# Optimization experiments

Hardware: AMD Instinct MI355X
Metric: run time of the kernel (lower is better)

## Reference

```python
import jax, jax.numpy as jnp
import numpy as np

N = 100000   # nodes
E = 1600000  # edges
D_IN = 128
H = 64
L = 3        # num SAGE layers
G = 512      # graphs in batch


def setup_inputs() -> dict:
    key = jax.random.key(0)
    ks = jax.random.split(key, 12)
    s = 0.05
    return {
        "x": jax.random.normal(ks[0], (N, D_IN), dtype=jnp.float32),
        "edge_index": jax.random.randint(ks[1], (2, E), 0, N, dtype=jnp.int64),
        "edge_attr": jax.random.normal(ks[2], (E, 1), dtype=jnp.float32),
        "batch": jnp.sort(jax.random.randint(ks[3], (N,), 0, G, dtype=jnp.int64)),
        "W0": jax.random.normal(ks[4], (D_IN, H), dtype=jnp.float32) * s,
        "b0": jnp.zeros((H,), dtype=jnp.float32),
        "Wl": jax.random.normal(ks[5], (L, H, H), dtype=jnp.float32) * s,  # lin_l (aggregated neighbors), has bias
        "bl": jnp.zeros((L, H), dtype=jnp.float32),
        "Wr": jax.random.normal(ks[6], (L, H, H), dtype=jnp.float32) * s,  # lin_r (root), no bias
        "W1": jax.random.normal(ks[7], (H, H), dtype=jnp.float32) * s,
        "b1": jnp.zeros((H,), dtype=jnp.float32),
    }


def reference(x, edge_index, edge_attr, batch, W0, b0, Wl, bl, Wr, W1, b1):
    # edge_attr is accepted but unused, matching the torch module.
    h = jax.nn.relu(x @ W0 + b0)                    # [N, H]
    src, dst = edge_index[0], edge_index[1]
    ones_e = jnp.ones((E,), dtype=h.dtype)
    deg = jax.ops.segment_sum(ones_e, dst, num_segments=N)
    deg = jnp.clip(deg, 1.0)[:, None]               # avoid div by zero (PyG mean -> 0 for isolated)
    for i in range(L):
        # SAGEConv: mean-aggregate source features onto targets, then lin_l(agg)+lin_r(h)
        agg = jax.ops.segment_sum(h[src], dst, num_segments=N) / deg  # [N, H]
        h = jax.nn.relu(agg @ Wl[i] + bl[i] + h @ Wr[i])
    # global_mean_pool over batch ids
    cnt = jax.ops.segment_sum(jnp.ones((N,), dtype=h.dtype), batch, num_segments=G)
    pooled = jax.ops.segment_sum(h, batch, num_segments=G) / jnp.clip(cnt, 1.0)[:, None]  # [G, H]
    return pooled @ W1 + b1                          # [G, H]
```

## Files before the change

### kernel.cpp

```cpp
#include <hip/hip_runtime.h>
#include <hip/hip_bf16.h>

#define NN 100000
#define NE 1600000
#define DIN 128
#define NG 512
#define MAXD 64
#define NBUK 391
#define BCAP 5120
#define CHUNK ((NE + NBUK - 1) / NBUK)
#define NTILE ((NN + 63) >> 6)

typedef __attribute__((ext_vector_type(8))) __bf16 bf16x8;
typedef __attribute__((ext_vector_type(4))) float f32x4;

static __device__ __forceinline__ unsigned short bfhi(float f) {
    __hip_bfloat16 h = __float2bfloat16(f);
    return *reinterpret_cast<unsigned short*>(&h);
}
static __device__ __forceinline__ float bf2f(unsigned short u) {
    unsigned v = (unsigned)u << 16;
    return __uint_as_float(v);
}
static __device__ __forceinline__ bf16x8 ldfrag(const unsigned short* p) {
    bf16x8 r;
    __builtin_memcpy(&r, p, 16);
    return r;
}


#define GB 256
__global__ void __launch_bounds__(512) k_front(const int* __restrict__ src,
                                               const int* __restrict__ dst,
                                               int* __restrict__ cursor,
                                               unsigned int* __restrict__ bucket,
                                               const float* __restrict__ x,
                                               const float* __restrict__ W0,
                                               const float* __restrict__ b0,
                                               float* __restrict__ h) {
    __shared__ unsigned short sA0[16 * 64 * 8];
    __shared__ unsigned short sA1[16 * 64 * 8];
    __shared__ unsigned short sB0[16 * 64 * 8];
    __shared__ unsigned short sB1[16 * 64 * 8];
    __shared__ int lcnt[NBUK];
    __shared__ int lbase[NBUK];
    if (blockIdx.x < NBUK) {
        for (int i = threadIdx.x; i < NBUK; i += 512) lcnt[i] = 0;
        __syncthreads();
        int e0 = blockIdx.x * CHUNK;
        int e1 = min(e0 + CHUNK, NE);
        for (int e = e0 + (int)threadIdx.x; e < e1; e += 512)
            atomicAdd(&lcnt[dst[e] >> 8], 1);
        __syncthreads();
        for (int i = threadIdx.x; i < NBUK; i += 512) {
            int c = lcnt[i];
            lbase[i] = c ? atomicAdd(&cursor[i], c) : 0;
            lcnt[i] = 0;
        }
        __syncthreads();
        for (int e = e0 + (int)threadIdx.x; e < e1; e += 512) {
            int d = dst[e];
            int s = src[e];
            int bk = d >> 8;
            int pos = lbase[bk] + atomicAdd(&lcnt[bk], 1);
            if (pos < BCAP)
                bucket[(size_t)bk * BCAP + pos] = ((unsigned)s << 8) | (unsigned)(d & 255);
        }
    } else {
        for (int i = threadIdx.x; i < 8192; i += 512) {
            int k = i >> 6, c = i & 63;
            int slot = ((k >> 5) << 2) | (c >> 4);
            int ln   = (((k >> 3) & 3) << 4) | (c & 15);
            int addr = (((slot << 6) | ln) << 3) | (k & 7);
            float w0 = W0[i];
            unsigned short hh = bfhi(w0);
            sB0[addr] = hh;
            sB1[addr] = bfhi(w0 - bf2f(hh));
        }
        int lane = threadIdx.x & 63;
        int wv   = threadIdx.x >> 6;
        int cb   = wv & 3;
        int rbh  = wv >> 2;
        int col  = (cb << 4) | (lane & 15);
        float bj = b0[col];
        int r0   = (lane >> 4) << 2;
        for (int t = blockIdx.x - NBUK; t < NTILE; t += GB) {
            int n0 = t << 6;
            __syncthreads();
#pragma unroll
            for (int i = 0; i < 4; ++i) {
                int tau = (int)threadIdx.x + (i << 9);
                int r = tau >> 5, kq = tau & 31;
                int n = n0 + r;
                float4 v = make_float4(0.f, 0.f, 0.f, 0.f);
                if (n < NN) v = *(const float4*)(x + ((size_t)n << 7) + (kq << 2));
                int k0   = kq << 2;
                int slot = ((k0 >> 5) << 2) | (r >> 4);
                int ln   = (((k0 >> 3) & 3) << 4) | (r & 15);
                int base = (((slot << 6) | ln) << 3) | (k0 & 7);
                unsigned short h0 = bfhi(v.x), h1 = bfhi(v.y),
                               h2 = bfhi(v.z), h3 = bfhi(v.w);
                *(ushort4*)(&sA0[base]) = make_ushort4(h0, h1, h2, h3);
                *(ushort4*)(&sA1[base]) = make_ushort4(
                    bfhi(v.x - bf2f(h0)), bfhi(v.y - bf2f(h1)),
                    bfhi(v.z - bf2f(h2)), bfhi(v.w - bf2f(h3)));
            }
            __syncthreads();
            f32x4 acc[2] = {{0.f,0.f,0.f,0.f},{0.f,0.f,0.f,0.f}};
#pragma unroll
            for (int ks = 0; ks < 4; ++ks) {
                int bbase = ((((ks << 2) | cb) << 6) | lane) << 3;
                bf16x8 bh = ldfrag(&sB0[bbase]);
                bf16x8 bl_ = ldfrag(&sB1[bbase]);
#pragma unroll
                for (int rl = 0; rl < 2; ++rl) {
                    int rb = (rbh << 1) | rl;
                    int abase = ((((ks << 2) | rb) << 6) | lane) << 3;
                    bf16x8 ah = ldfrag(&sA0[abase]);
                    bf16x8 al = ldfrag(&sA1[abase]);
                    acc[rl] = __builtin_amdgcn_mfma_f32_16x16x32_bf16(ah, bh,  acc[rl], 0, 0, 0);
                    acc[rl] = __builtin_amdgcn_mfma_f32_16x16x32_bf16(ah, bl_, acc[rl], 0, 0, 0);
                    acc[rl] = __builtin_amdgcn_mfma_f32_16x16x32_bf16(al, bh,  acc[rl], 0, 0, 0);
                }
            }
#pragma unroll
            for (int rl = 0; rl < 2; ++rl) {
                int rb = (rbh << 1) | rl;
#pragma unroll
                for (int reg = 0; reg < 4; ++reg) {
                    int row = (rb << 4) + r0 + reg;
                    int n = n0 + row;
                    if (n < NN)
                        h[((size_t)n << 6) + col] = fmaxf(acc[rl][reg] + bj, 0.f);
                }
            }
        }
    }
}

__device__ __forceinline__ void gemmLR_mfma(unsigned short* sA0, unsigned short* sA1,
                                            unsigned short* sBL0, unsigned short* sBL1,
                                            unsigned short* sBR0, unsigned short* sBR1,
                                            int tid, int nblk, int bidx,
                                            float* __restrict__ h_r,
                                            __hip_bfloat16* __restrict__ g,
                                            const float* __restrict__ Wl,
                                            const float* __restrict__ bl,
                                            const float* __restrict__ Wr) {
    for (int i = tid; i < 4096; i += 256) {
        int k = i >> 6, c = i & 63;
        int slot = ((k >> 5) << 2) | (c >> 4);
        int ln   = (((k >> 3) & 3) << 4) | (c & 15);
        int addr = (((slot << 6) | ln) << 3) | (k & 7);
        float wl = Wl[i];
        unsigned short hl = bfhi(wl);
        sBL0[addr] = hl;
        sBL1[addr] = bfhi(wl - bf2f(hl));
        float wr = Wr[i];
        unsigned short hr = bfhi(wr);
        sBR0[addr] = hr;
        sBR1[addr] = bfhi(wr - bf2f(hr));
    }
    int lane = tid & 63;
    int cb   = tid >> 6;
    int col  = (cb << 4) | (lane & 15);
    float bj = bl[col];
    int r0   = (lane >> 4) << 2;
    unsigned short* gp = (unsigned short*)g;
    for (int t = bidx; t < NTILE; t += nblk) {
        int n0 = t << 6;
        __syncthreads();
#pragma unroll
        for (int i = 0; i < 4; ++i) {
            int tau = tid + (i << 8);
            int r = tau >> 4, kq = tau & 15;
            int n = n0 + r;
            float4 v = make_float4(0.f, 0.f, 0.f, 0.f);
            if (n < NN) v = *(const float4*)(h_r + ((size_t)n << 6) + (kq << 2));
            int k0   = kq << 2;
            int slot = ((k0 >> 5) << 2) | (r >> 4);
            int ln   = (((k0 >> 3) & 3) << 4) | (r & 15);
            int base = (((slot << 6) | ln) << 3) | (k0 & 7);
            unsigned short h0 = bfhi(v.x), h1 = bfhi(v.y),
                           h2 = bfhi(v.z), h3 = bfhi(v.w);
            *(ushort4*)(&sA0[base]) = make_ushort4(h0, h1, h2, h3);
            *(ushort4*)(&sA1[base]) = make_ushort4(
                bfhi(v.x - bf2f(h0)), bfhi(v.y - bf2f(h1)),
                bfhi(v.z - bf2f(h2)), bfhi(v.w - bf2f(h3)));
        }
        __syncthreads();
        f32x4 accl[4] = {{0.f,0.f,0.f,0.f},{0.f,0.f,0.f,0.f},
                         {0.f,0.f,0.f,0.f},{0.f,0.f,0.f,0.f}};
        f32x4 accr[4] = {{0.f,0.f,0.f,0.f},{0.f,0.f,0.f,0.f},
                         {0.f,0.f,0.f,0.f},{0.f,0.f,0.f,0.f}};
#pragma unroll
        for (int ks = 0; ks < 2; ++ks) {
            int bbase = ((((ks << 2) | cb) << 6) | lane) << 3;
            bf16x8 bLh = ldfrag(&sBL0[bbase]);
            bf16x8 bLl = ldfrag(&sBL1[bbase]);
            bf16x8 bRh = ldfrag(&sBR0[bbase]);
            bf16x8 bRl = ldfrag(&sBR1[bbase]);
#pragma unroll
            for (int rb = 0; rb < 4; ++rb) {
                int abase = ((((ks << 2) | rb) << 6) | lane) << 3;
                bf16x8 ah = ldfrag(&sA0[abase]);
                bf16x8 al = ldfrag(&sA1[abase]);
                accl[rb] = __builtin_amdgcn_mfma_f32_16x16x32_bf16(ah, bLh, accl[rb], 0, 0, 0);
                accl[rb] = __builtin_amdgcn_mfma_f32_16x16x32_bf16(ah, bLl, accl[rb], 0, 0, 0);
                accl[rb] = __builtin_amdgcn_mfma_f32_16x16x32_bf16(al, bLh, accl[rb], 0, 0, 0);
                accr[rb] = __builtin_amdgcn_mfma_f32_16x16x32_bf16(ah, bRh, accr[rb], 0, 0, 0);
                accr[rb] = __builtin_amdgcn_mfma_f32_16x16x32_bf16(ah, bRl, accr[rb], 0, 0, 0);
                accr[rb] = __builtin_amdgcn_mfma_f32_16x16x32_bf16(al, bRh, accr[rb], 0, 0, 0);
            }
        }
#pragma unroll
        for (int rb = 0; rb < 4; ++rb) {
#pragma unroll
            for (int reg = 0; reg < 4; ++reg) {
                int row = (rb << 4) + r0 + reg;
                int n = n0 + row;
                if (n < NN) {
                    size_t o = ((size_t)n << 6) + col;
                    gp[o]  = bfhi(accl[rb][reg]);
                    h_r[o] = accr[rb][reg] + bj;
                }
            }
        }
    }
}

#define MGB 512
__global__ void __launch_bounds__(256) k_mid(const unsigned int* __restrict__ bucket,
                                             const int* __restrict__ cursor,
                                             int* __restrict__ cnt,
                                             int* __restrict__ ell,
                                             float* __restrict__ h_r,
                                             __hip_bfloat16* __restrict__ g,
                                             const float* __restrict__ Wl,
                                             const float* __restrict__ bl,
                                             const float* __restrict__ Wr) {
    __shared__ unsigned short sA0[8 * 64 * 8];
    __shared__ unsigned short sA1[8 * 64 * 8];
    __shared__ unsigned short sBL0[8 * 64 * 8];
    __shared__ unsigned short sBL1[8 * 64 * 8];
    __shared__ unsigned short sBR0[8 * 64 * 8];
    __shared__ unsigned short sBR1[8 * 64 * 8];
    __shared__ int lc[256];
    if (blockIdx.x < NBUK) {
        lc[threadIdx.x] = 0;
        int b = blockIdx.x;
        int4* ep = (int4*)(ell + (((size_t)b << 8) * MAXD));
        for (int i = threadIdx.x; i < (256 * MAXD) / 4; i += 256)
            ep[i] = make_int4(NN, NN, NN, NN);
        __syncthreads();
        int m = min(cursor[b], BCAP);
        const unsigned int* bp = bucket + (size_t)b * BCAP;
        for (int i = threadIdx.x; i < m; i += 256) {
            unsigned v = bp[i];
            int dlo = (int)(v & 255u);
            int s   = (int)(v >> 8);
            int p   = atomicAdd(&lc[dlo], 1);
            if (p < MAXD)
                ell[(((size_t)b << 8) + dlo) * MAXD + p] = s;
        }
        __syncthreads();
        int n = (b << 8) + (int)threadIdx.x;
        if (n < NN) cnt[n] = lc[threadIdx.x];
    } else {
        gemmLR_mfma(sA0, sA1, sBL0, sBL1, sBR0, sBR1,
                    threadIdx.x, MGB, blockIdx.x - NBUK, h_r, g, Wl, bl, Wr);
    }
}

__global__ void __launch_bounds__(256) k_gemmLR(float* __restrict__ h_r,
                                                __hip_bfloat16* __restrict__ g,
                                                const float* __restrict__ Wl,
                                                const float* __restrict__ bl,
                                                const float* __restrict__ Wr) {
    __shared__ unsigned short sA0[8 * 64 * 8];
    __shared__ unsigned short sA1[8 * 64 * 8];
    __shared__ unsigned short sBL0[8 * 64 * 8];
    __shared__ unsigned short sBL1[8 * 64 * 8];
    __shared__ unsigned short sBR0[8 * 64 * 8];
    __shared__ unsigned short sBR1[8 * 64 * 8];
    gemmLR_mfma(sA0, sA1, sBL0, sBL1, sBR0, sBR1,
                threadIdx.x, gridDim.x, blockIdx.x, h_r, g, Wl, bl, Wr);
}

__global__ void __launch_bounds__(256) k_gather(const unsigned int* __restrict__ g2,
                                                float* __restrict__ r_h,
                                                const int* __restrict__ cnt,
                                                const int* __restrict__ ell) {
    int lane = threadIdx.x & 63;
    int half = lane >> 5;
    int col  = lane & 31;
    int wv = __builtin_amdgcn_readfirstlane((int)((blockIdx.x * 256 + threadIdx.x) >> 6));
    int nw = (gridDim.x * 256) >> 6;
    for (int p = wv; p < NN / 2; p += nw) {
        int nA = 2 * p, nB = nA + 1;
        int dgA = cnt[nA], dgB = cnt[nB];
        int myn  = half ? nB : nA;
        int mydg = half ? dgB : dgA;
        int maxd = min(max(dgA, dgB), MAXD);
        int iters = (maxd + 7) & ~7;
        int idx0 = ell[(size_t)myn * MAXD + col];
        int idx1 = NN;
        if (iters > 32) idx1 = ell[(size_t)myn * MAXD + 32 + col];
        float L0=0.f,L1=0.f,L2=0.f,L3=0.f,L4=0.f,L5=0.f,L6=0.f,L7=0.f;
        float H0=0.f,H1=0.f,H2=0.f,H3=0.f,H4=0.f,H5=0.f,H6=0.f,H7=0.f;
        int it0 = min(iters, 32);
        for (int j = 0; j < it0; j += 8) {
            int i0 = __shfl(idx0, half * 32 + j);
            int i1 = __shfl(idx0, half * 32 + j + 1);
            int i2 = __shfl(idx0, half * 32 + j + 2);
            int i3 = __shfl(idx0, half * 32 + j + 3);
            int i4 = __shfl(idx0, half * 32 + j + 4);
            int i5 = __shfl(idx0, half * 32 + j + 5);
            int i6 = __shfl(idx0, half * 32 + j + 6);
            int i7 = __shfl(idx0, half * 32 + j + 7);
            unsigned u0 = g2[(size_t)i0 * 32 + col];
            unsigned u1 = g2[(size_t)i1 * 32 + col];
            unsigned u2 = g2[(size_t)i2 * 32 + col];
            unsigned u3 = g2[(size_t)i3 * 32 + col];
            unsigned u4 = g2[(size_t)i4 * 32 + col];
            unsigned u5 = g2[(size_t)i5 * 32 + col];
            unsigned u6 = g2[(size_t)i6 * 32 + col];
            unsigned u7 = g2[(size_t)i7 * 32 + col];
            L0 += __uint_as_float(u0 << 16); H0 += __uint_as_float(u0 & 0xffff0000u);
            L1 += __uint_as_float(u1 << 16); H1 += __uint_as_float(u1 & 0xffff0000u);
            L2 += __uint_as_float(u2 << 16); H2 += __uint_as_float(u2 & 0xffff0000u);
            L3 += __uint_as_float(u3 << 16); H3 += __uint_as_float(u3 & 0xffff0000u);
            L4 += __uint_as_float(u4 << 16); H4 += __uint_as_float(u4 & 0xffff0000u);
            L5 += __uint_as_float(u5 << 16); H5 += __uint_as_float(u5 & 0xffff0000u);
            L6 += __uint_as_float(u6 << 16); H6 += __uint_as_float(u6 & 0xffff0000u);
            L7 += __uint_as_float(u7 << 16); H7 += __uint_as_float(u7 & 0xffff0000u);
        }
        for (int j = 0; j < iters - 32; j += 8) {
            int i0 = __shfl(idx1, half * 32 + j);
            int i1 = __shfl(idx1, half * 32 + j + 1);
            int i2 = __shfl(idx1, half * 32 + j + 2);
            int i3 = __shfl(idx1, half * 32 + j + 3);
            int i4 = __shfl(idx1, half * 32 + j + 4);
            int i5 = __shfl(idx1, half * 32 + j + 5);
            int i6 = __shfl(idx1, half * 32 + j + 6);
            int i7 = __shfl(idx1, half * 32 + j + 7);
            unsigned u0 = g2[(size_t)i0 * 32 + col];
            unsigned u1 = g2[(size_t)i1 * 32 + col];
            unsigned u2 = g2[(size_t)i2 * 32 + col];
            unsigned u3 = g2[(size_t)i3 * 32 + col];
            unsigned u4 = g2[(size_t)i4 * 32 + col];
            unsigned u5 = g2[(size_t)i5 * 32 + col];
            unsigned u6 = g2[(size_t)i6 * 32 + col];
            unsigned u7 = g2[(size_t)i7 * 32 + col];
            L0 += __uint_as_float(u0 << 16); H0 += __uint_as_float(u0 & 0xffff0000u);
            L1 += __uint_as_float(u1 << 16); H1 += __uint_as_float(u1 & 0xffff0000u);
            L2 += __uint_as_float(u2 << 16); H2 += __uint_as_float(u2 & 0xffff0000u);
            L3 += __uint_as_float(u3 << 16); H3 += __uint_as_float(u3 & 0xffff0000u);
            L4 += __uint_as_float(u4 << 16); H4 += __uint_as_float(u4 & 0xffff0000u);
            L5 += __uint_as_float(u5 << 16); H5 += __uint_as_float(u5 & 0xffff0000u);
            L6 += __uint_as_float(u6 << 16); H6 += __uint_as_float(u6 & 0xffff0000u);
            L7 += __uint_as_float(u7 << 16); H7 += __uint_as_float(u7 & 0xffff0000u);
        }
        float inv  = 1.0f / fmaxf((float)mydg, 1.0f);
        float sumL = ((L0 + L1) + (L2 + L3)) + ((L4 + L5) + (L6 + L7));
        float sumH = ((H0 + H1) + (H2 + H3)) + ((H4 + H5) + (H6 + H7));
        float2* rp = (float2*)r_h + (size_t)myn * 32 + col;
        float2 rv = *rp;
        rv.x = fmaxf(fmaf(sumL, inv, rv.x), 0.0f);
        rv.y = fmaxf(fmaf(sumH, inv, rv.y), 0.0f);
        *rp = rv;
    }
}

__global__ void __launch_bounds__(256) k_pool(const int* __restrict__ batch,
                                              const float* __restrict__ h,
                                              float* __restrict__ pool,
                                              float* __restrict__ cntg) {
    int lane = threadIdx.x & 63;
    int wid  = (blockIdx.x * 256 + threadIdx.x) >> 6;
    int nw   = (gridDim.x * 256) >> 6;
    int chunk = (NN + nw - 1) / nw;
    int n0 = wid * chunk;
    if (n0 >= NN) return;
    int n1 = min(n0 + chunk, NN);
    int cur = batch[n0];
    float acc = 0.0f, acc_c = 0.0f;
    for (int n = n0; n < n1; ++n) {
        int b = batch[n];
        if (b != cur) {
            atomicAdd(&pool[(size_t)cur * 64 + lane], acc);
            if (lane == 0) atomicAdd(&cntg[cur], acc_c);
            acc = 0.0f; acc_c = 0.0f; cur = b;
        }
        acc   += h[(size_t)n * 64 + lane];
        acc_c += 1.0f;
    }
    atomicAdd(&pool[(size_t)cur * 64 + lane], acc);
    if (lane == 0) atomicAdd(&cntg[cur], acc_c);
}

__global__ void __launch_bounds__(256) k_out(const float* __restrict__ pool,
                                             const float* __restrict__ cntg,
                                             const float* __restrict__ W1,
                                             const float* __restrict__ b1,
                                             float* __restrict__ out) {
    __shared__ float sW[64 * 64];
    for (int i = threadIdx.x; i < 64 * 64; i += 256) sW[i] = W1[i];
    __syncthreads();
    int lane = threadIdx.x & 63;
    int wid  = (blockIdx.x * 256 + threadIdx.x) >> 6;
    int nw   = (gridDim.x * 256) >> 6;
    for (int gidx = wid; gidx < NG; gidx += nw) {
        float ic = 1.0f / fmaxf(cntg[gidx], 1.0f);
        float acc = 0.0f;
#pragma unroll
        for (int k = 0; k < 64; ++k)
            acc = fmaf(pool[(size_t)gidx * 64 + k], sW[k * 64 + lane], acc);
        out[(size_t)gidx * 64 + lane] = fmaf(acc, ic, b1[lane]);
    }
}

extern "C" void kernel_launch(void* const* d_in, const int* in_sizes, int n_in,
                              void* d_out, int out_size, void* d_ws, size_t ws_size,
                              hipStream_t stream) {
    const float* x     = (const float*)d_in[0];
    const int*   ei    = (const int*)d_in[1];
    const int*   batch = (const int*)d_in[3];
    const float* W0    = (const float*)d_in[4];
    const float* b0    = (const float*)d_in[5];
    const float* Wl    = (const float*)d_in[6];
    const float* bl    = (const float*)d_in[7];
    const float* Wr    = (const float*)d_in[8];
    const float* W1    = (const float*)d_in[9];
    const float* b1    = (const float*)d_in[10];
    float* out = (float*)d_out;

    char* ws = (char*)d_ws;
    size_t off = 0;
    auto alloc = [&](size_t bytes) -> void* {
        void* p = ws + off;
        off += (bytes + 255) & ~(size_t)255;
        return p;
    };
    float*          A      = (float*)alloc((size_t)NN * 64 * 4);
    __hip_bfloat16* G      = (__hip_bfloat16*)alloc((size_t)NN * 64 * 2);
    size_t zstart = off;
    (void)alloc((size_t)MAXD * 2);
    int*   cursor = (int*)alloc((size_t)NBUK * 4);
    float* pool   = (float*)alloc((size_t)NG * 64 * 4);
    float* cntg   = (float*)alloc((size_t)NG * 4);
    size_t zlen = off - zstart;
    int*          ell    = (int*)alloc((size_t)NBUK * 256 * MAXD * 4);
    unsigned int* bucket = (unsigned int*)alloc((size_t)NBUK * BCAP * 4);
    int*          cnt    = (int*)alloc((size_t)NN * 4);

    const int* src = ei;
    const int* dst = ei + NE;

    hipMemsetAsync(ws + zstart, 0, zlen, stream);

    k_front<<<NBUK + GB, 512, 0, stream>>>(src, dst, cursor, bucket, x, W0, b0, A);
    k_mid<<<NBUK + MGB, 256, 0, stream>>>(bucket, cursor, cnt, ell, A, G,
                                          Wl, bl, Wr);
    k_gather<<<4096, 256, 0, stream>>>((const unsigned int*)G, A, cnt, ell);

    for (int l = 1; l < 3; ++l) {
        k_gemmLR<<<512, 256, 0, stream>>>(A, G,
                                          Wl + (size_t)l * 64 * 64,
                                          bl + (size_t)l * 64,
                                          Wr + (size_t)l * 64 * 64);
        k_gather<<<4096, 256, 0, stream>>>((const unsigned int*)G, A, cnt, ell);
    }

    k_pool<<<256, 256, 0, stream>>>(batch, A, pool, cntg);
    k_out<<<128, 256, 0, stream>>>(pool, cntg, W1, b1, out);
}
```

Measured before the change: 388.3 us.

## Swizzle LDS MFMA fragments and gather four nodes per wave with 8-byte loads

```diff
diff --git a/kernel.cpp b/kernel.cpp
--- a/kernel.cpp
+++ b/kernel.cpp
@@ -22,10 +22,13 @@
     unsigned v = (unsigned)u << 16;
     return __uint_as_float(v);
 }
-static __device__ __forceinline__ bf16x8 ldfrag(const unsigned short* p) {
+static __device__ __forceinline__ bf16x8 ldfrag(const void* p) {
     bf16x8 r;
     __builtin_memcpy(&r, p, 16);
     return r;
+}
+static __device__ __forceinline__ int swz(int a) {
+    return a ^ (((a >> 8) & 3) << 5) ^ (((a >> 12) & 3) << 4);
 }
 
 
@@ -71,11 +74,11 @@
             int k = i >> 6, c = i & 63;
             int slot = ((k >> 5) << 2) | (c >> 4);
             int ln   = (((k >> 3) & 3) << 4) | (c & 15);
-            int addr = (((slot << 6) | ln) << 3) | (k & 7);
+            int ba   = swz((((((slot << 6) | ln) << 3) | (k & 7)) << 1));
             float w0 = W0[i];
             unsigned short hh = bfhi(w0);
-            sB0[addr] = hh;
-            sB1[addr] = bfhi(w0 - bf2f(hh));
+            *(unsigned short*)((char*)sB0 + ba) = hh;
+            *(unsigned short*)((char*)sB1 + ba) = bfhi(w0 - bf2f(hh));
         }
         int lane = threadIdx.x & 63;
         int wv   = threadIdx.x >> 6;
@@ -97,11 +100,11 @@
                 int k0   = kq << 2;
                 int slot = ((k0 >> 5) << 2) | (r >> 4);
                 int ln   = (((k0 >> 3) & 3) << 4) | (r & 15);
-                int base = (((slot << 6) | ln) << 3) | (k0 & 7);
+                int ba   = swz((((((slot << 6) | ln) << 3) | (k0 & 7)) << 1));
                 unsigned short h0 = bfhi(v.x), h1 = bfhi(v.y),
                                h2 = bfhi(v.z), h3 = bfhi(v.w);
-                *(ushort4*)(&sA0[base]) = make_ushort4(h0, h1, h2, h3);
-                *(ushort4*)(&sA1[base]) = make_ushort4(
+                *(ushort4*)((char*)sA0 + ba) = make_ushort4(h0, h1, h2, h3);
+                *(ushort4*)((char*)sA1 + ba) = make_ushort4(
                     bfhi(v.x - bf2f(h0)), bfhi(v.y - bf2f(h1)),
                     bfhi(v.z - bf2f(h2)), bfhi(v.w - bf2f(h3)));
             }
@@ -109,15 +112,15 @@
             f32x4 acc[2] = {{0.f,0.f,0.f,0.f},{0.f,0.f,0.f,0.f}};
 #pragma unroll
             for (int ks = 0; ks < 4; ++ks) {
-                int bbase = ((((ks << 2) | cb) << 6) | lane) << 3;
-                bf16x8 bh = ldfrag(&sB0[bbase]);
-                bf16x8 bl_ = ldfrag(&sB1[bbase]);
+                int bb = swz(((((ks << 2) | cb) << 6) | lane) << 4);
+                bf16x8 bh  = ldfrag((const char*)sB0 + bb);
+                bf16x8 bl_ = ldfrag((const char*)sB1 + bb);
 #pragma unroll
                 for (int rl = 0; rl < 2; ++rl) {
                     int rb = (rbh << 1) | rl;
-                    int abase = ((((ks << 2) | rb) << 6) | lane) << 3;
-                    bf16x8 ah = ldfrag(&sA0[abase]);
-                    bf16x8 al = ldfrag(&sA1[abase]);
+                    int ab = swz(((((ks << 2) | rb) << 6) | lane) << 4);
+                    bf16x8 ah = ldfrag((const char*)sA0 + ab);
+                    bf16x8 al = ldfrag((const char*)sA1 + ab);
                     acc[rl] = __builtin_amdgcn_mfma_f32_16x16x32_bf16(ah, bh,  acc[rl], 0, 0, 0);
                     acc[rl] = __builtin_amdgcn_mfma_f32_16x16x32_bf16(ah, bl_, acc[rl], 0, 0, 0);
                     acc[rl] = __builtin_amdgcn_mfma_f32_16x16x32_bf16(al, bh,  acc[rl], 0, 0, 0);
@@ -151,15 +154,15 @@
         int k = i >> 6, c = i & 63;
         int slot = ((k >> 5) << 2) | (c >> 4);
         int ln   = (((k >> 3) & 3) << 4) | (c & 15);
-        int addr = (((slot << 6) | ln) << 3) | (k & 7);
+        int ba   = swz((((((slot << 6) | ln) << 3) | (k & 7)) << 1));
         float wl = Wl[i];
         unsigned short hl = bfhi(wl);
-        sBL0[addr] = hl;
-        sBL1[addr] = bfhi(wl - bf2f(hl));
+        *(unsigned short*)((char*)sBL0 + ba) = hl;
+        *(unsigned short*)((char*)sBL1 + ba) = bfhi(wl - bf2f(hl));
         float wr = Wr[i];
         unsigned short hr = bfhi(wr);
-        sBR0[addr] = hr;
-        sBR1[addr] = bfhi(wr - bf2f(hr));
+        *(unsigned short*)((char*)sBR0 + ba) = hr;
+        *(unsigned short*)((char*)sBR1 + ba) = bfhi(wr - bf2f(hr));
     }
     int lane = tid & 63;
     int cb   = tid >> 6;
@@ -180,11 +183,11 @@
             int k0   = kq << 2;
             int slot = ((k0 >> 5) << 2) | (r >> 4);
             int ln   = (((k0 >> 3) & 3) << 4) | (r & 15);
-            int base = (((slot << 6) | ln) << 3) | (k0 & 7);
+            int ba   = swz((((((slot << 6) | ln) << 3) | (k0 & 7)) << 1));
             unsigned short h0 = bfhi(v.x), h1 = bfhi(v.y),
                            h2 = bfhi(v.z), h3 = bfhi(v.w);
-            *(ushort4*)(&sA0[base]) = make_ushort4(h0, h1, h2, h3);
-            *(ushort4*)(&sA1[base]) = make_ushort4(
+            *(ushort4*)((char*)sA0 + ba) = make_ushort4(h0, h1, h2, h3);
+            *(ushort4*)((char*)sA1 + ba) = make_ushort4(
                 bfhi(v.x - bf2f(h0)), bfhi(v.y - bf2f(h1)),
                 bfhi(v.z - bf2f(h2)), bfhi(v.w - bf2f(h3)));
         }
@@ -195,16 +198,16 @@
                          {0.f,0.f,0.f,0.f},{0.f,0.f,0.f,0.f}};
 #pragma unroll
         for (int ks = 0; ks < 2; ++ks) {
-            int bbase = ((((ks << 2) | cb) << 6) | lane) << 3;
-            bf16x8 bLh = ldfrag(&sBL0[bbase]);
-            bf16x8 bLl = ldfrag(&sBL1[bbase]);
-            bf16x8 bRh = ldfrag(&sBR0[bbase]);
-            bf16x8 bRl = ldfrag(&sBR1[bbase]);
+            int bb = swz(((((ks << 2) | cb) << 6) | lane) << 4);
+            bf16x8 bLh = ldfrag((const char*)sBL0 + bb);
+            bf16x8 bLl = ldfrag((const char*)sBL1 + bb);
+            bf16x8 bRh = ldfrag((const char*)sBR0 + bb);
+            bf16x8 bRl = ldfrag((const char*)sBR1 + bb);
 #pragma unroll
             for (int rb = 0; rb < 4; ++rb) {
-                int abase = ((((ks << 2) | rb) << 6) | lane) << 3;
-                bf16x8 ah = ldfrag(&sA0[abase]);
-                bf16x8 al = ldfrag(&sA1[abase]);
+                int ab = swz(((((ks << 2) | rb) << 6) | lane) << 4);
+                bf16x8 ah = ldfrag((const char*)sA0 + ab);
+                bf16x8 al = ldfrag((const char*)sA1 + ab);
                 accl[rb] = __builtin_amdgcn_mfma_f32_16x16x32_bf16(ah, bLh, accl[rb], 0, 0, 0);
                 accl[rb] = __builtin_amdgcn_mfma_f32_16x16x32_bf16(ah, bLl, accl[rb], 0, 0, 0);
                 accl[rb] = __builtin_amdgcn_mfma_f32_16x16x32_bf16(al, bLh, accl[rb], 0, 0, 0);
@@ -287,87 +290,68 @@
                 threadIdx.x, gridDim.x, blockIdx.x, h_r, g, Wl, bl, Wr);
 }
 
-__global__ void __launch_bounds__(256) k_gather(const unsigned int* __restrict__ g2,
+__global__ void __launch_bounds__(256) k_gather(const uint2* __restrict__ g2,
                                                 float* __restrict__ r_h,
                                                 const int* __restrict__ cnt,
                                                 const int* __restrict__ ell) {
     int lane = threadIdx.x & 63;
-    int half = lane >> 5;
-    int col  = lane & 31;
+    int q    = lane >> 4;
+    int c16  = lane & 15;
     int wv = __builtin_amdgcn_readfirstlane((int)((blockIdx.x * 256 + threadIdx.x) >> 6));
     int nw = (gridDim.x * 256) >> 6;
-    for (int p = wv; p < NN / 2; p += nw) {
-        int nA = 2 * p, nB = nA + 1;
-        int dgA = cnt[nA], dgB = cnt[nB];
-        int myn  = half ? nB : nA;
-        int mydg = half ? dgB : dgA;
-        int maxd = min(max(dgA, dgB), MAXD);
+    for (int p = wv; p < NN / 4; p += nw) {
+        int n0  = 4 * p;
+        int myn = n0 + q;
+        int d   = cnt[myn];
+        int dm  = max(d, __shfl_xor(d, 16));
+        dm      = max(dm, __shfl_xor(dm, 32));
+        int maxd  = min(dm, MAXD);
         int iters = (maxd + 7) & ~7;
-        int idx0 = ell[(size_t)myn * MAXD + col];
-        int idx1 = NN;
-        if (iters > 32) idx1 = ell[(size_t)myn * MAXD + 32 + col];
-        float L0=0.f,L1=0.f,L2=0.f,L3=0.f,L4=0.f,L5=0.f,L6=0.f,L7=0.f;
-        float H0=0.f,H1=0.f,H2=0.f,H3=0.f,H4=0.f,H5=0.f,H6=0.f,H7=0.f;
-        int it0 = min(iters, 32);
-        for (int j = 0; j < it0; j += 8) {
-            int i0 = __shfl(idx0, half * 32 + j);
-            int i1 = __shfl(idx0, half * 32 + j + 1);
-            int i2 = __shfl(idx0, half * 32 + j + 2);
-            int i3 = __shfl(idx0, half * 32 + j + 3);
-            int i4 = __shfl(idx0, half * 32 + j + 4);
-            int i5 = __shfl(idx0, half * 32 + j + 5);
-            int i6 = __shfl(idx0, half * 32 + j + 6);
-            int i7 = __shfl(idx0, half * 32 + j + 7);
-            unsigned u0 = g2[(size_t)i0 * 32 + col];
-            unsigned u1 = g2[(size_t)i1 * 32 + col];
-            unsigned u2 = g2[(size_t)i2 * 32 + col];
-            unsigned u3 = g2[(size_t)i3 * 32 + col];
-            unsigned u4 = g2[(size_t)i4 * 32 + col];
-            unsigned u5 = g2[(size_t)i5 * 32 + col];
-            unsigned u6 = g2[(size_t)i6 * 32 + col];
-            unsigned u7 = g2[(size_t)i7 * 32 + col];
-            L0 += __uint_as_float(u0 << 16); H0 += __uint_as_float(u0 & 0xffff0000u);
-            L1 += __uint_as_float(u1 << 16); H1 += __uint_as_float(u1 & 0xffff0000u);
-            L2 += __uint_as_float(u2 << 16); H2 += __uint_as_float(u2 & 0xffff0000u);
-            L3 += __uint_as_float(u3 << 16); H3 += __uint_as_float(u3 & 0xffff0000u);
-            L4 += __uint_as_float(u4 << 16); H4 += __uint_as_float(u4 & 0xffff0000u);
-            L5 += __uint_as_float(u5 << 16); H5 += __uint_as_float(u5 & 0xffff0000u);
-            L6 += __uint_as_float(u6 << 16); H6 += __uint_as_float(u6 & 0xffff0000u);
-            L7 += __uint_as_float(u7 << 16); H7 += __uint_as_float(u7 & 0xffff0000u);
-        }
-        for (int j = 0; j < iters - 32; j += 8) {
-            int i0 = __shfl(idx1, half * 32 + j);
-            int i1 = __shfl(idx1, half * 32 + j + 1);
-            int i2 = __shfl(idx1, half * 32 + j + 2);
-            int i3 = __shfl(idx1, half * 32 + j + 3);
-            int i4 = __shfl(idx1, half * 32 + j + 4);
-            int i5 = __shfl(idx1, half * 32 + j + 5);
-            int i6 = __shfl(idx1, half * 32 + j + 6);
-            int i7 = __shfl(idx1, half * 32 + j + 7);
-            unsigned u0 = g2[(size_t)i0 * 32 + col];
-            unsigned u1 = g2[(size_t)i1 * 32 + col];
-            unsigned u2 = g2[(size_t)i2 * 32 + col];
-            unsigned u3 = g2[(size_t)i3 * 32 + col];
-            unsigned u4 = g2[(size_t)i4 * 32 + col];
-            unsigned u5 = g2[(size_t)i5 * 32 + col];
-            unsigned u6 = g2[(size_t)i6 * 32 + col];
-            unsigned u7 = g2[(size_t)i7 * 32 + col];
-            L0 += __uint_as_float(u0 << 16); H0 += __uint_as_float(u0 & 0xffff0000u);
-            L1 += __uint_as_float(u1 << 16); H1 += __uint_as_float(u1 & 0xffff0000u);
-            L2 += __uint_as_float(u2 << 16); H2 += __uint_as_float(u2 & 0xffff0000u);
-            L3 += __uint_as_float(u3 << 16); H3 += __uint_as_float(u3 & 0xffff0000u);
-            L4 += __uint_as_float(u4 << 16); H4 += __uint_as_float(u4 & 0xffff0000u);
-            L5 += __uint_as_float(u5 << 16); H5 += __uint_as_float(u5 & 0xffff0000u);
-            L6 += __uint_as_float(u6 << 16); H6 += __uint_as_float(u6 & 0xffff0000u);
-            L7 += __uint_as_float(u7 << 16); H7 += __uint_as_float(u7 & 0xffff0000u);
-        }
-        float inv  = 1.0f / fmaxf((float)mydg, 1.0f);
-        float sumL = ((L0 + L1) + (L2 + L3)) + ((L4 + L5) + (L6 + L7));
-        float sumH = ((H0 + H1) + (H2 + H3)) + ((H4 + H5) + (H6 + H7));
-        float2* rp = (float2*)r_h + (size_t)myn * 32 + col;
-        float2 rv = *rp;
-        rv.x = fmaxf(fmaf(sumL, inv, rv.x), 0.0f);
-        rv.y = fmaxf(fmaf(sumH, inv, rv.y), 0.0f);
+        int4 ld = *(const int4*)(ell + ((size_t)myn << 6) + (c16 << 2));
+        float a0=0.f, a1=0.f, a2=0.f, a3=0.f;
+        float e0=0.f, e1=0.f, e2=0.f, e3=0.f;
+        for (int j0 = 0; j0 < iters; j0 += 8) {
+            int s0 = (q << 4) | (j0 >> 2);
+            int i0 = __shfl(ld.x, s0);
+            int i1 = __shfl(ld.y, s0);
+            int i2 = __shfl(ld.z, s0);
+            int i3 = __shfl(ld.w, s0);
+            int i4 = __shfl(ld.x, s0 + 1);
+            int i5 = __shfl(ld.y, s0 + 1);
+            int i6 = __shfl(ld.z, s0 + 1);
+            int i7 = __shfl(ld.w, s0 + 1);
+            uint2 u0 = g2[(size_t)i0 * 16 + c16];
+            uint2 u1 = g2[(size_t)i1 * 16 + c16];
+            uint2 u2 = g2[(size_t)i2 * 16 + c16];
+            uint2 u3 = g2[(size_t)i3 * 16 + c16];
+            uint2 u4 = g2[(size_t)i4 * 16 + c16];
+            uint2 u5 = g2[(size_t)i5 * 16 + c16];
+            uint2 u6 = g2[(size_t)i6 * 16 + c16];
+            uint2 u7 = g2[(size_t)i7 * 16 + c16];
+            a0 += __uint_as_float(u0.x << 16); a1 += __uint_as_float(u0.x & 0xffff0000u);
+            a2 += __uint_as_float(u0.y << 16); a3 += __uint_as_float(u0.y & 0xffff0000u);
+            e0 += __uint_as_float(u1.x << 16); e1 += __uint_as_float(u1.x & 0xffff0000u);
+            e2 += __uint_as_float(u1.y << 16); e3 += __uint_as_float(u1.y & 0xffff0000u);
+            a0 += __uint_as_float(u2.x << 16); a1 += __uint_as_float(u2.x & 0xffff0000u);
+            a2 += __uint_as_float(u2.y << 16); a3 += __uint_as_float(u2.y & 0xffff0000u);
+            e0 += __uint_as_float(u3.x << 16); e1 += __uint_as_float(u3.x & 0xffff0000u);
+            e2 += __uint_as_float(u3.y << 16); e3 += __uint_as_float(u3.y & 0xffff0000u);
+            a0 += __uint_as_float(u4.x << 16); a1 += __uint_as_float(u4.x & 0xffff0000u);
+            a2 += __uint_as_float(u4.y << 16); a3 += __uint_as_float(u4.y & 0xffff0000u);
+            e0 += __uint_as_float(u5.x << 16); e1 += __uint_as_float(u5.x & 0xffff0000u);
+            e2 += __uint_as_float(u5.y << 16); e3 += __uint_as_float(u5.y & 0xffff0000u);
+            a0 += __uint_as_float(u6.x << 16); a1 += __uint_as_float(u6.x & 0xffff0000u);
+            a2 += __uint_as_float(u6.y << 16); a3 += __uint_as_float(u6.y & 0xffff0000u);
+            e0 += __uint_as_float(u7.x << 16); e1 += __uint_as_float(u7.x & 0xffff0000u);
+            e2 += __uint_as_float(u7.y << 16); e3 += __uint_as_float(u7.y & 0xffff0000u);
+        }
+        float inv = 1.0f / fmaxf((float)d, 1.0f);
+        float4* rp = (float4*)r_h + ((size_t)myn << 4) + c16;
+        float4 rv = *rp;
+        rv.x = fmaxf(fmaf(a0 + e0, inv, rv.x), 0.0f);
+        rv.y = fmaxf(fmaf(a1 + e1, inv, rv.y), 0.0f);
+        rv.z = fmaxf(fmaf(a2 + e2, inv, rv.z), 0.0f);
+        rv.w = fmaxf(fmaf(a3 + e3, inv, rv.w), 0.0f);
         *rp = rv;
     }
 }
@@ -462,14 +446,14 @@
     k_front<<<NBUK + GB, 512, 0, stream>>>(src, dst, cursor, bucket, x, W0, b0, A);
     k_mid<<<NBUK + MGB, 256, 0, stream>>>(bucket, cursor, cnt, ell, A, G,
                                           Wl, bl, Wr);
-    k_gather<<<4096, 256, 0, stream>>>((const unsigned int*)G, A, cnt, ell);
+    k_gather<<<4096, 256, 0, stream>>>((const uint2*)G, A, cnt, ell);
 
     for (int l = 1; l < 3; ++l) {
         k_gemmLR<<<512, 256, 0, stream>>>(A, G,
                                           Wl + (size_t)l * 64 * 64,
                                           bl + (size_t)l * 64,
                                           Wr + (size_t)l * 64 * 64);
-        k_gather<<<4096, 256, 0, stream>>>((const unsigned int*)G, A, cnt, ell);
+        k_gather<<<4096, 256, 0, stream>>>((const uint2*)G, A, cnt, ell);
     }
 
     k_pool<<<256, 256, 0, stream>>>(batch, A, pool, cntg);
```

Result: no change. 394.2 us (+1.5%).
